# Optimization experiments

Hardware: AMD Instinct MI355X
Metric: run time of the kernel (lower is better)

Reference implementation:

```python
import jax, jax.numpy as jnp
import numpy as np

N = 100000   # nodes
E = 600000   # edges
D = 128      # input = hidden = output dim
L = 3        # GNN layers
C = 40       # num_classes
EPS = 1e-5   # BatchNorm eps


def setup_inputs() -> dict:
    key = jax.random.key(0)
    ks = jax.random.split(key, 8)
    x = jax.random.normal(ks[0], (N, D), jnp.float32)
    edge_index = jax.random.randint(ks[1], (2, E), 0, N, jnp.int32)
    # GCNConv weights per layer (Glorot-ish scale), bias zeros
    Ws = jax.random.normal(ks[2], (L, D, D), jnp.float32) / np.sqrt(D)
    bs = jnp.zeros((L, D), jnp.float32)
    # BatchNorm affine params
    gammas = jnp.ones((L, D), jnp.float32)
    betas = jnp.zeros((L, D), jnp.float32)
    # PReLU single slope per layer (torch default init 0.25)
    prelu_a = jnp.full((L,), 0.25, jnp.float32)
    # classification head: Linear(D,D) -> ReLU -> Linear(D,C)
    Wh1 = jax.random.normal(ks[3], (D, D), jnp.float32) / np.sqrt(D)
    bh1 = jnp.zeros((D,), jnp.float32)
    Wh2 = jax.random.normal(ks[4], (D, C), jnp.float32) / np.sqrt(D)
    bh2 = jnp.zeros((C,), jnp.float32)
    return dict(x=x, edge_index=edge_index, Ws=Ws, bs=bs, gammas=gammas,
                betas=betas, prelu_a=prelu_a, Wh1=Wh1, bh1=bh1, Wh2=Wh2, bh2=bh2)


def _gcn_conv(h, src, dst, norm, W, b):
    # PyG GCNConv: out_i = sum_{j->i} norm_ij * (x_j W) + b  (self-loops already in src/dst)
    m = (h @ W)[src] * norm[:, None]          # [E+N, D_out]
    return jax.ops.segment_sum(m, dst, num_segments=N) + b


def reference(x, edge_index, Ws, bs, gammas, betas, prelu_a, Wh1, bh1, Wh2, bh2):
    # add self-loops + symmetric normalization (computed once; same graph each layer)
    loops = jnp.arange(N, dtype=edge_index.dtype)
    src = jnp.concatenate([edge_index[0], loops])
    dst = jnp.concatenate([edge_index[1], loops])
    deg = jax.ops.segment_sum(jnp.ones_like(dst, jnp.float32), dst, num_segments=N)
    dinv = jax.lax.rsqrt(jnp.maximum(deg, 1.0))  # deg >= 1 thanks to self-loops
    norm = dinv[src] * dinv[dst]                 # [E+N]

    h = x
    for l in range(L):
        h = _gcn_conv(h, src, dst, norm, Ws[l], bs[l])
        # BatchNorm in training mode: batch statistics over nodes
        mu = h.mean(axis=0)
        var = h.var(axis=0)
        h = (h - mu) * jax.lax.rsqrt(var + EPS) * gammas[l] + betas[l]
        # PReLU
        h = jnp.where(h > 0, h, prelu_a[l] * h)

    embeddings = h
    logits = jax.nn.relu(embeddings @ Wh1 + bh1) @ Wh2 + bh2
    out = jnp.argmax(logits, axis=1)
    return embeddings, logits, out
```

## Files before the change

### kernel.cpp

```cpp
#include <hip/hip_runtime.h>
#include <hip/hip_bf16.h>
#include <cstddef>

#define N_NODES 100000
#define N_EDGES 600000
#define DD 128
#define LL 3
#define CC 40
#define BN_EPS 1e-5f

__device__ __forceinline__ float ldf(const void* p, long i, int f32) {
    return f32 ? ((const float*)p)[i] : __bfloat162float(((const __hip_bfloat16*)p)[i]);
}
__device__ __forceinline__ void stf(void* p, long i, float v, int f32) {
    if (f32) ((float*)p)[i] = v;
    else     ((__hip_bfloat16*)p)[i] = __float2bfloat16(v);
}

__global__ __launch_bounds__(256) void k_detect(const void* __restrict__ x, int* __restrict__ dflag) {
    __shared__ int s[256];
    int t = threadIdx.x;
    const __hip_bfloat16* xb = (const __hip_bfloat16*)x;
    int bad = 0;
    for (int i = t; i < 4096; i += 256) {
        float v = __bfloat162float(xb[i]);
        float a = fabsf(v);
        if (!(a < 1e6f)) bad++;
        else if (v != 0.f && a < 1e-30f) bad++;
    }
    s[t] = bad; __syncthreads();
    for (int off = 128; off > 0; off >>= 1) {
        if (t < off) s[t] += s[t + off];
        __syncthreads();
    }
    if (t == 0) *dflag = (s[0] > 64) ? 1 : 0;
}


__global__ __launch_bounds__(256) void k_init(int* cnt, int* fpos, int* rowptr, float* stats) {
    int i = blockIdx.x * 256 + threadIdx.x;
    if (i < N_NODES) { cnt[i] = 0; fpos[i] = 0; }
    if (i < 6 * DD) stats[i] = 0.f;
    if (i == 0) rowptr[N_NODES] = N_EDGES;
}

__global__ __launch_bounds__(256) void k_count(const int* __restrict__ ei, int* __restrict__ cnt) {
    int e = blockIdx.x * 256 + threadIdx.x;
    if (e < N_EDGES) atomicAdd(&cnt[ei[N_EDGES + e]], 1);
}

__global__ __launch_bounds__(256) void k_scan1(const int* __restrict__ cnt, int* __restrict__ rowptr,
                                               int* __restrict__ bsum, float* __restrict__ dinv) {
    __shared__ int s[256];
    int t = threadIdx.x;
    int i = blockIdx.x * 256 + t;
    int v = (i < N_NODES) ? cnt[i] : 0;
    if (i < N_NODES) dinv[i] = 1.f / sqrtf((float)(1 + v));
    s[t] = v; __syncthreads();
    for (int off = 1; off < 256; off <<= 1) {
        int x = (t >= off) ? s[t - off] : 0;
        __syncthreads();
        s[t] += x; __syncthreads();
    }
    if (i < N_NODES) rowptr[i] = s[t] - v;
    if (t == 255) bsum[blockIdx.x] = s[255];
}

__global__ __launch_bounds__(512) void k_scan2(int* bsum, int nb) {
    __shared__ int s[512];
    int t = threadIdx.x;
    int v = (t < nb) ? bsum[t] : 0;
    s[t] = v; __syncthreads();
    for (int off = 1; off < 512; off <<= 1) {
        int x = (t >= off) ? s[t - off] : 0;
        __syncthreads();
        s[t] += x; __syncthreads();
    }
    if (t < nb) bsum[t] = s[t] - v;
}

__global__ __launch_bounds__(256) void k_scan3(int* rowptr, const int* __restrict__ bsum) {
    int i = blockIdx.x * 256 + threadIdx.x;
    if (i < N_NODES) rowptr[i] += bsum[blockIdx.x];
}

__global__ __launch_bounds__(256) void k_fill(const int* __restrict__ ei, int* __restrict__ fpos,
                                              const int* __restrict__ rowptr, int* __restrict__ adj) {
    int e = blockIdx.x * 256 + threadIdx.x;
    if (e < N_EDGES) {
        int d = ei[N_EDGES + e];
        int p = atomicAdd(&fpos[d], 1);
        adj[rowptr[d] + p] = ei[e];
    }
}

__device__ __forceinline__ void load_act(const void* __restrict__ src, long row, int lane, int f,
                                         const float* __restrict__ bnp,
                                         float s0, float s1, float h0, float h1, float al,
                                         float& o0, float& o1) {
    if (bnp) {
        float2 v = ((const float2*)src)[row * 64 + lane];
        float y0 = fmaf(v.x, s0, h0), y1 = fmaf(v.y, s1, h1);
        o0 = (y0 > 0.f) ? y0 : al * y0;
        o1 = (y1 > 0.f) ? y1 : al * y1;
    } else if (f) {
        float2 v = ((const float2*)src)[row * 64 + lane];
        o0 = v.x; o1 = v.y;
    } else {
        unsigned u = ((const unsigned*)src)[row * 64 + lane];
        o0 = __uint_as_float(u << 16);
        o1 = __uint_as_float(u & 0xffff0000u);
    }
}


__global__ __launch_bounds__(256) void k_agg(const void* __restrict__ src,
                                             const int* __restrict__ rowptr,
                                             const int* __restrict__ adj,
                                             const float* __restrict__ dinv,
                                             const float* __restrict__ bnp,
                                             float* __restrict__ outp,
                                             const int* __restrict__ dflag) {
    int f = *dflag;
    int lane = threadIdx.x & 63;
    int i = blockIdx.x * 4 + (threadIdx.x >> 6);
    if (i >= N_NODES) return;
    float s0 = 0.f, s1 = 0.f, h0 = 0.f, h1 = 0.f, al = 0.f;
    if (bnp) {
        s0 = bnp[2 * lane];       s1 = bnp[2 * lane + 1];
        h0 = bnp[128 + 2 * lane]; h1 = bnp[129 + 2 * lane];
        al = bnp[256];
    }
    float di = dinv[i];
    int e0 = rowptr[i], e1 = rowptr[i + 1];
    float x0, x1;
    load_act(src, i, lane, f, bnp, s0, s1, h0, h1, al, x0, x1);
    float acc0 = di * x0, acc1 = di * x1;

    for (int base = e0; base < e1; base += 64) {
        int m = e1 - base; if (m > 64) m = 64;
        int aj = (lane < m) ? adj[base + lane] : 0;
        float djl = (lane < m) ? dinv[aj] : 0.f;
        int t = 0;
        for (; t + 2 <= m; t += 2) {
            int j0 = __shfl(aj, t), j1 = __shfl(aj, t + 1);
            float d0 = __shfl(djl, t), d1 = __shfl(djl, t + 1);
            float p0, p1, q0, q1;
            load_act(src, j0, lane, f, bnp, s0, s1, h0, h1, al, p0, p1);
            load_act(src, j1, lane, f, bnp, s0, s1, h0, h1, al, q0, q1);
            acc0 += d0 * p0 + d1 * q0;
            acc1 += d0 * p1 + d1 * q1;
        }
        if (t < m) {
            int j0 = __shfl(aj, t);
            float d0 = __shfl(djl, t);
            float p0, p1;
            load_act(src, j0, lane, f, bnp, s0, s1, h0, h1, al, p0, p1);
            acc0 += d0 * p0;
            acc1 += d0 * p1;
        }
    }
    float2 r; r.x = di * acc0; r.y = di * acc1;
    ((float2*)outp)[(size_t)i * 64 + lane] = r;
}


__global__ __launch_bounds__(256, 4) void k_gemm2(const float* __restrict__ A,
                                                  const void* __restrict__ W, long woff,
                                                  const void* __restrict__ bias, long boff,
                                                  const float* __restrict__ bnpA,
                                                  float* __restrict__ stats,
                                                  float* __restrict__ Cout, int relu,
                                                  const int* __restrict__ dflag) {
    __shared__ float Wl[128][64];
    __shared__ float sred[16][64];
    int f = *dflag;
    int tid = threadIdx.x;
    int rowbase = (blockIdx.x >> 1) * 128;
    int colbase = (blockIdx.x & 1) * 64;

    if (f) {
        const float4* W4 = (const float4*)W + (woff >> 2);
        for (int u = tid; u < 128 * 16; u += 256) {
            int k = u >> 4, cq = u & 15;
            *(float4*)&Wl[k][cq * 4] = W4[k * 32 + (colbase >> 2) + cq];
        }
    } else {
        const unsigned* Wb = (const unsigned*)((const __hip_bfloat16*)W + woff);
        for (int u = tid; u < 128 * 32; u += 256) {
            int k = u >> 5, c2 = u & 31;
            unsigned v = Wb[k * 64 + (colbase >> 1) + c2];
            Wl[k][c2 * 2]     = __uint_as_float(v << 16);
            Wl[k][c2 * 2 + 1] = __uint_as_float(v & 0xffff0000u);
        }
    }
    __syncthreads();

    int tx = tid & 15;
    int ty = tid >> 4;
    int r0 = rowbase + ty * 8;
    float acc[8][4];
    #pragma unroll
    for (int i = 0; i < 8; ++i)
        #pragma unroll
        for (int j = 0; j < 4; ++j) acc[i][j] = 0.f;

    const float4* A4 = (const float4*)A;
    bool full = (rowbase + 128) <= N_NODES;
    float alA = bnpA ? bnpA[256] : 0.f;

    for (int k4 = 0; k4 < 32; ++k4) {
        float a[8][4];
        if (full) {
            #pragma unroll
            for (int i = 0; i < 8; ++i)
                *(float4*)a[i] = A4[(long)(r0 + i) * 32 + k4];
        } else {
            #pragma unroll
            for (int i = 0; i < 8; ++i) {
                float4 v = make_float4(0.f, 0.f, 0.f, 0.f);
                if (r0 + i < N_NODES) v = A4[(long)(r0 + i) * 32 + k4];
                *(float4*)a[i] = v;
            }
        }
        if (bnpA) {
            float4 s4 = ((const float4*)bnpA)[k4];
            float4 h4 = ((const float4*)(bnpA + 128))[k4];
            float sv[4] = {s4.x, s4.y, s4.z, s4.w};
            float hv[4] = {h4.x, h4.y, h4.z, h4.w};
            #pragma unroll
            for (int i = 0; i < 8; ++i)
                #pragma unroll
                for (int kk = 0; kk < 4; ++kk) {
                    float y = fmaf(a[i][kk], sv[kk], hv[kk]);
                    a[i][kk] = (y > 0.f) ? y : alA * y;
                }
        }
        #pragma unroll
        for (int kk = 0; kk < 4; ++kk) {
            float4 w = *(const float4*)&Wl[k4 * 4 + kk][tx * 4];
            #pragma unroll
            for (int i = 0; i < 8; ++i) {
                acc[i][0] += a[i][kk] * w.x;
                acc[i][1] += a[i][kk] * w.y;
                acc[i][2] += a[i][kk] * w.z;
                acc[i][3] += a[i][kk] * w.w;
            }
        }
    }

    float b4[4] = {0.f, 0.f, 0.f, 0.f};
    if (bias) {
        #pragma unroll
        for (int j = 0; j < 4; ++j) b4[j] = ldf(bias, boff + colbase + tx * 4 + j, f);
    }
    float ls[4] = {0.f, 0.f, 0.f, 0.f};
    float lq[4] = {0.f, 0.f, 0.f, 0.f};
    #pragma unroll
    for (int i = 0; i < 8; ++i) {
        int r = r0 + i;
        if (r < N_NODES) {
            float o[4];
            #pragma unroll
            for (int j = 0; j < 4; ++j) {
                float v = acc[i][j] + b4[j];
                if (relu) v = fmaxf(v, 0.f);
                o[j] = v;
                ls[j] += v;
                lq[j] += v * v;
            }
            *(float4*)&Cout[(long)r * 128 + colbase + tx * 4] = make_float4(o[0], o[1], o[2], o[3]);
        }
    }
    if (stats) {
        #pragma unroll
        for (int j = 0; j < 4; ++j) sred[ty][tx * 4 + j] = ls[j];
        __syncthreads();
        if (tid < 64) {
            float t = 0.f;
            #pragma unroll
            for (int g = 0; g < 16; ++g) t += sred[g][tid];
            atomicAdd(&stats[colbase + tid], t);
        }
        __syncthreads();
        #pragma unroll
        for (int j = 0; j < 4; ++j) sred[ty][tx * 4 + j] = lq[j];
        __syncthreads();
        if (tid < 64) {
            float t = 0.f;
            #pragma unroll
            for (int g = 0; g < 16; ++g) t += sred[g][tid];
            atomicAdd(&stats[128 + colbase + tid], t);
        }
    }
}

__global__ __launch_bounds__(128) void k_bnprep(const float* __restrict__ stats,
                                                const void* __restrict__ g, const void* __restrict__ b,
                                                const void* __restrict__ a, int l,
                                                float* __restrict__ bnp, const int* __restrict__ dflag) {
    int f = *dflag;
    int c = threadIdx.x;
    float mean = stats[c] / (float)N_NODES;
    float var = stats[128 + c] / (float)N_NODES - mean * mean;
    float inv = 1.f / sqrtf(var + BN_EPS);
    float s = ldf(g, (long)l * DD + c, f) * inv;
    bnp[c] = s;
    bnp[128 + c] = ldf(b, (long)l * DD + c, f) - mean * s;
    if (c == 0) bnp[256] = ldf(a, l, f);
}

__global__ __launch_bounds__(256) void k_emb(const float* __restrict__ H, const float* __restrict__ bnp,
                                             void* __restrict__ out, const int* __restrict__ dflag) {
    int f = *dflag;
    long idx = (long)blockIdx.x * 256 + threadIdx.x;
    int c = (int)(idx & 127);
    float al = bnp[256];
    float y = fmaf(H[idx], bnp[c], bnp[128 + c]);
    y = (y > 0.f) ? y : al * y;
    stf(out, idx, y, f);
}


__global__ __launch_bounds__(256) void k_head(const float* __restrict__ Hd, const void* __restrict__ W2,
                                              const void* __restrict__ b2,
                                              void* __restrict__ out_base,
                                              const int* __restrict__ dflag) {
    __shared__ float Wl[128][40];
    __shared__ float bl[40];
    __shared__ float rv[32][8];
    __shared__ int ri[32][8];
    int f = *dflag;
    int tid = threadIdx.x;
    for (int u = tid; u < 128 * 40; u += 256) Wl[u / 40][u % 40] = ldf(W2, u, f);
    if (tid < 40) bl[tid] = ldf(b2, tid, f);
    __syncthreads();
    int rl = tid >> 3, g = tid & 7;
    long r = (long)blockIdx.x * 32 + rl;
    float acc[5];
    #pragma unroll
    for (int j = 0; j < 5; ++j) acc[j] = bl[g * 5 + j];
    for (int k = 0; k < 128; ++k) {
        float h = Hd[r * 128 + k];
        #pragma unroll
        for (int j = 0; j < 5; ++j) acc[j] += h * Wl[k][g * 5 + j];
    }
    float best = acc[0]; int bi = 0;
    #pragma unroll
    for (int j = 1; j < 5; ++j)
        if (acc[j] > best) { best = acc[j]; bi = j; }
    const long LOG_OFF = (long)N_NODES * DD;
    const long ARG_OFF = (long)N_NODES * (DD + CC);
    #pragma unroll
    for (int j = 0; j < 5; ++j) stf(out_base, LOG_OFF + r * 40 + g * 5 + j, acc[j], f);
    rv[rl][g] = best; ri[rl][g] = g * 5 + bi;
    __syncthreads();
    if (tid < 32) {
        long row = (long)blockIdx.x * 32 + tid;
        float bb = rv[tid][0]; int bbi = ri[tid][0];
        #pragma unroll
        for (int g2 = 1; g2 < 8; ++g2)
            if (rv[tid][g2] > bb) { bb = rv[tid][g2]; bbi = ri[tid][g2]; }
        stf(out_base, ARG_OFF + row, (float)bbi, f);
    }
}


extern "C" void kernel_launch(void* const* d_in, const int* in_sizes, int n_in,
                              void* d_out, int out_size, void* d_ws, size_t ws_size,
                              hipStream_t stream) {
    const void* x   = d_in[0];
    const int* ei   = (const int*)d_in[1];
    const void* Ws  = d_in[2];
    const void* bs  = d_in[3];
    const void* gam = d_in[4];
    const void* bet = d_in[5];
    const void* pa  = d_in[6];
    const void* Wh1 = d_in[7];
    const void* bh1 = d_in[8];
    const void* Wh2 = d_in[9];
    const void* bh2 = d_in[10];

    char* w = (char*)d_ws;
    int* cnt     = (int*)w;    w += sizeof(int) * N_NODES;
    int* fpos    = (int*)w;    w += sizeof(int) * N_NODES;
    int* rowptr  = (int*)w;    w += sizeof(int) * (N_NODES + 4);
    int* adj     = (int*)w;    w += sizeof(int) * N_EDGES;
    int* bsum    = (int*)w;    w += sizeof(int) * 512;
    int* dflag   = (int*)w;    w += sizeof(int) * 4;
    float* dinv  = (float*)w;  w += sizeof(float) * N_NODES;
    float* stats = (float*)w;  w += sizeof(float) * (6 * DD);
    float* bnp   = (float*)w;  w += sizeof(float) * (3 * 512);
    float* bufA  = (float*)w;  w += sizeof(float) * (size_t)N_NODES * DD;
    float* bufB  = (float*)w;  w += sizeof(float) * (size_t)N_NODES * DD;

    const int scanBlocks = (N_NODES + 255) / 256;
    const int edgeBlocks = (N_EDGES + 255) / 256;
    const int elemBlocks = (N_NODES * DD) / 256;
    const int gemmBlocks = ((N_NODES + 127) / 128) * 2;
    const int aggBlocks  = (N_NODES + 3) / 4;

    k_detect<<<1, 256, 0, stream>>>(x, dflag);
    k_init<<<scanBlocks, 256, 0, stream>>>(cnt, fpos, rowptr, stats);
    k_count<<<edgeBlocks, 256, 0, stream>>>(ei, cnt);
    k_scan1<<<scanBlocks, 256, 0, stream>>>(cnt, rowptr, bsum, dinv);
    k_scan2<<<1, 512, 0, stream>>>(bsum, scanBlocks);
    k_scan3<<<scanBlocks, 256, 0, stream>>>(rowptr, bsum);
    k_fill<<<edgeBlocks, 256, 0, stream>>>(ei, fpos, rowptr, adj);

    for (int l = 0; l < LL; ++l) {
        const void* src = (l == 0) ? x : (const void*)bufB;
        const float* bn = (l == 0) ? nullptr : (bnp + (l - 1) * 512);
        k_agg<<<aggBlocks, 256, 0, stream>>>(src, rowptr, adj, dinv, bn, bufA, dflag);
        k_gemm2<<<gemmBlocks, 256, 0, stream>>>(bufA, Ws, (long)l * DD * DD, bs, (long)l * DD,
                                                nullptr, stats + l * 256, bufB, 0, dflag);
        k_bnprep<<<1, 128, 0, stream>>>(stats + l * 256, gam, bet, pa, l, bnp + l * 512, dflag);
    }

    k_emb<<<elemBlocks, 256, 0, stream>>>(bufB, bnp + 2 * 512, d_out, dflag);
    k_gemm2<<<gemmBlocks, 256, 0, stream>>>(bufB, Wh1, 0, bh1, 0, bnp + 2 * 512,
                                            nullptr, bufA, 1, dflag);
    k_head<<<(N_NODES / 32), 256, 0, stream>>>(bufA, Wh2, bh2, d_out, dflag);
}
```

Baseline: 777.4 us.

## Move dense GEMMs onto bf16 MFMA with three-way split for fp32 accuracy

The 128x128 dense matmuls in each GCN layer and the head now run on bf16 MFMA instructions instead of scalar fp32 FMAs. Each operand is split into hi/mid/lo bf16 parts and six cross products are accumulated, keeping results close to fp32. A new pre-pass kernel packs all four weight matrices once into the MFMA fragment layout, so the GEMM just copies them into shared memory. Each block now covers all 128 output columns, which changes stats reduction and occupancy. The cost is six times the MFMA work, extra conversion ALU work on activations, and scalar (non-vectorised) output stores.

```diff
diff --git a/kernel.cpp b/kernel.cpp
--- a/kernel.cpp
+++ b/kernel.cpp
@@ -9,12 +9,24 @@
 #define CC 40
 #define BN_EPS 1e-5f
 
+typedef __attribute__((ext_vector_type(8))) short bfrag;
+typedef __attribute__((ext_vector_type(4))) float f32x4;
+
 __device__ __forceinline__ float ldf(const void* p, long i, int f32) {
     return f32 ? ((const float*)p)[i] : __bfloat162float(((const __hip_bfloat16*)p)[i]);
 }
 __device__ __forceinline__ void stf(void* p, long i, float v, int f32) {
     if (f32) ((float*)p)[i] = v;
     else     ((__hip_bfloat16*)p)[i] = __float2bfloat16(v);
+}
+
+__device__ __forceinline__ unsigned short f2bf(float f) {
+    unsigned u = __float_as_uint(f);
+    unsigned r = (u + 0x7fffu + ((u >> 16) & 1u)) >> 16;
+    return (unsigned short)r;
+}
+__device__ __forceinline__ float bf2f(unsigned short h) {
+    return __uint_as_float(((unsigned)h) << 16);
 }
 
 __global__ __launch_bounds__(256) void k_detect(const void* __restrict__ x, int* __restrict__ dflag) {
@@ -34,6 +46,28 @@
         __syncthreads();
     }
     if (t == 0) *dflag = (s[0] > 64) ? 1 : 0;
+}
+
+__global__ __launch_bounds__(256) void k_packw(const void* __restrict__ Ws, const void* __restrict__ Wh1,
+                                               unsigned short* __restrict__ Wp,
+                                               const int* __restrict__ dflag) {
+    int f = *dflag;
+    int u = blockIdx.x * 256 + threadIdx.x;
+    int mat = u >> 14;
+    int r = u & 16383;
+    int k = r >> 7, c = r & 127;
+    float wv = (mat < 3) ? ldf(Ws, (long)mat * 16384 + r, f) : ldf(Wh1, r, f);
+    unsigned short hi = f2bf(wv);
+    float r1 = wv - bf2f(hi);
+    unsigned short mid = f2bf(r1);
+    float r2 = r1 - bf2f(mid);
+    unsigned short lo = f2bf(r2);
+    int n = c >> 4, ks = k >> 5, j = k & 7;
+    int lanep = (c & 15) | (((k >> 3) & 3) << 4);
+    long base = (long)mat * 49152 + (long)((n * 4 + ks) * 3) * 512 + lanep * 8 + j;
+    Wp[base] = hi;
+    Wp[base + 512] = mid;
+    Wp[base + 1024] = lo;
 }
 
 
@@ -165,133 +199,176 @@
 }
 
 
-__global__ __launch_bounds__(256, 4) void k_gemm2(const float* __restrict__ A,
-                                                  const void* __restrict__ W, long woff,
+__global__ __launch_bounds__(256, 2) void k_gemm2(const float* __restrict__ A,
+                                                  const unsigned short* __restrict__ Wp,
                                                   const void* __restrict__ bias, long boff,
                                                   const float* __restrict__ bnpA,
                                                   float* __restrict__ stats,
                                                   float* __restrict__ Cout, int relu,
                                                   const int* __restrict__ dflag) {
-    __shared__ float Wl[128][64];
-    __shared__ float sred[16][64];
+    __shared__ unsigned short Wl[24576];
     int f = *dflag;
     int tid = threadIdx.x;
-    int rowbase = (blockIdx.x >> 1) * 128;
-    int colbase = (blockIdx.x & 1) * 64;
-
-    if (f) {
-        const float4* W4 = (const float4*)W + (woff >> 2);
-        for (int u = tid; u < 128 * 16; u += 256) {
-            int k = u >> 4, cq = u & 15;
-            *(float4*)&Wl[k][cq * 4] = W4[k * 32 + (colbase >> 2) + cq];
-        }
-    } else {
-        const unsigned* Wb = (const unsigned*)((const __hip_bfloat16*)W + woff);
-        for (int u = tid; u < 128 * 32; u += 256) {
-            int k = u >> 5, c2 = u & 31;
-            unsigned v = Wb[k * 64 + (colbase >> 1) + c2];
-            Wl[k][c2 * 2]     = __uint_as_float(v << 16);
-            Wl[k][c2 * 2 + 1] = __uint_as_float(v & 0xffff0000u);
-        }
-    }
-    __syncthreads();
-
-    int tx = tid & 15;
-    int ty = tid >> 4;
-    int r0 = rowbase + ty * 8;
-    float acc[8][4];
-    #pragma unroll
-    for (int i = 0; i < 8; ++i)
-        #pragma unroll
-        for (int j = 0; j < 4; ++j) acc[i][j] = 0.f;
-
+
+    int lane = tid & 63;
+    int w = tid >> 6;
+    int lr = lane & 15;
+    int lg = lane >> 4;
+    int rowbase = blockIdx.x * 128 + w * 32;
+
+    float bcol[8];
+    #pragma unroll
+    for (int n = 0; n < 8; ++n)
+        bcol[n] = bias ? ldf(bias, boff + n * 16 + lr, f) : 0.f;
+
+    float alA = bnpA ? bnpA[256] : 0.f;
+
+    bfrag ah[2][4], am[2][4], alo[2][4];
     const float4* A4 = (const float4*)A;
-    bool full = (rowbase + 128) <= N_NODES;
-    float alA = bnpA ? bnpA[256] : 0.f;
-
-    for (int k4 = 0; k4 < 32; ++k4) {
-        float a[8][4];
-        if (full) {
+    #pragma unroll
+    for (int ks = 0; ks < 4; ++ks) {
+        int k0 = ks * 32 + lg * 8;
+        float bs_[8], bh_[8];
+        if (bnpA) {
+            float4 sa = *(const float4*)&bnpA[k0];
+            float4 sb = *(const float4*)&bnpA[k0 + 4];
+            float4 ha = *(const float4*)&bnpA[128 + k0];
+            float4 hb = *(const float4*)&bnpA[128 + k0 + 4];
+            bs_[0] = sa.x; bs_[1] = sa.y; bs_[2] = sa.z; bs_[3] = sa.w;
+            bs_[4] = sb.x; bs_[5] = sb.y; bs_[6] = sb.z; bs_[7] = sb.w;
+            bh_[0] = ha.x; bh_[1] = ha.y; bh_[2] = ha.z; bh_[3] = ha.w;
+            bh_[4] = hb.x; bh_[5] = hb.y; bh_[6] = hb.z; bh_[7] = hb.w;
+        }
+        #pragma unroll
+        for (int s = 0; s < 2; ++s) {
+            int row = rowbase + s * 16 + lr;
+            float xv[8];
+            if (row < N_NODES) {
+                long bi = (long)row * 32 + (k0 >> 2);
+                float4 x0 = A4[bi], x1 = A4[bi + 1];
+                xv[0] = x0.x; xv[1] = x0.y; xv[2] = x0.z; xv[3] = x0.w;
+                xv[4] = x1.x; xv[5] = x1.y; xv[6] = x1.z; xv[7] = x1.w;
+            } else {
+                #pragma unroll
+                for (int e = 0; e < 8; ++e) xv[e] = 0.f;
+            }
+            if (bnpA) {
+                #pragma unroll
+                for (int e = 0; e < 8; ++e) {
+                    float y = fmaf(xv[e], bs_[e], bh_[e]);
+                    xv[e] = (y > 0.f) ? y : alA * y;
+                }
+            }
+            bfrag hfr, mfr, lfr;
             #pragma unroll
-            for (int i = 0; i < 8; ++i)
-                *(float4*)a[i] = A4[(long)(r0 + i) * 32 + k4];
-        } else {
+            for (int e = 0; e < 8; ++e) {
+                unsigned short hb2 = f2bf(xv[e]);
+                float r1 = xv[e] - bf2f(hb2);
+                unsigned short mb2 = f2bf(r1);
+                float r2 = r1 - bf2f(mb2);
+                hfr[e] = (short)hb2;
+                mfr[e] = (short)mb2;
+                lfr[e] = (short)f2bf(r2);
+            }
+            ah[s][ks] = hfr;
+            am[s][ks] = mfr;
+            alo[s][ks] = lfr;
+        }
+    }
+
+    f32x4 acc[2][8];
+    #pragma unroll
+    for (int s = 0; s < 2; ++s)
+        #pragma unroll
+        for (int n = 0; n < 8; ++n) acc[s][n] = (f32x4){0.f, 0.f, 0.f, 0.f};
+
+    #pragma unroll
+    for (int h = 0; h < 2; ++h) {
+        if (h) __syncthreads();
+        {
+            const uint4* srcp = (const uint4*)(Wp + (size_t)h * 24576);
+            uint4* dstp = (uint4*)Wl;
             #pragma unroll
-            for (int i = 0; i < 8; ++i) {
-                float4 v = make_float4(0.f, 0.f, 0.f, 0.f);
-                if (r0 + i < N_NODES) v = A4[(long)(r0 + i) * 32 + k4];
-                *(float4*)a[i] = v;
-            }
-        }
-        if (bnpA) {
-            float4 s4 = ((const float4*)bnpA)[k4];
-            float4 h4 = ((const float4*)(bnpA + 128))[k4];
-            float sv[4] = {s4.x, s4.y, s4.z, s4.w};
-            float hv[4] = {h4.x, h4.y, h4.z, h4.w};
+            for (int u = 0; u < 12; ++u) dstp[tid + 256 * u] = srcp[tid + 256 * u];
+        }
+        __syncthreads();
+
+        #pragma unroll
+        for (int nn = 0; nn < 4; ++nn) {
+            int n = h * 4 + nn;
+            bfrag bh[4], bm[4], bl[4];
             #pragma unroll
-            for (int i = 0; i < 8; ++i)
+            for (int ks = 0; ks < 4; ++ks) {
+                int base = ((nn * 4 + ks) * 3) * 512 + lane * 8;
+                bh[ks] = *(const bfrag*)&Wl[base];
+                bm[ks] = *(const bfrag*)&Wl[base + 512];
+                bl[ks] = *(const bfrag*)&Wl[base + 1024];
+            }
+            #pragma unroll
+            for (int ks = 0; ks < 4; ++ks) {
                 #pragma unroll
-                for (int kk = 0; kk < 4; ++kk) {
-                    float y = fmaf(a[i][kk], sv[kk], hv[kk]);
-                    a[i][kk] = (y > 0.f) ? y : alA * y;
+                for (int s = 0; s < 2; ++s) {
+                    acc[s][n] = __builtin_amdgcn_mfma_f32_16x16x32_bf16(ah[s][ks],  bh[ks], acc[s][n], 0, 0, 0);
+                    acc[s][n] = __builtin_amdgcn_mfma_f32_16x16x32_bf16(am[s][ks],  bh[ks], acc[s][n], 0, 0, 0);
+                    acc[s][n] = __builtin_amdgcn_mfma_f32_16x16x32_bf16(ah[s][ks],  bm[ks], acc[s][n], 0, 0, 0);
+                    acc[s][n] = __builtin_amdgcn_mfma_f32_16x16x32_bf16(am[s][ks],  bm[ks], acc[s][n], 0, 0, 0);
+                    acc[s][n] = __builtin_amdgcn_mfma_f32_16x16x32_bf16(alo[s][ks], bh[ks], acc[s][n], 0, 0, 0);
+                    acc[s][n] = __builtin_amdgcn_mfma_f32_16x16x32_bf16(ah[s][ks],  bl[ks], acc[s][n], 0, 0, 0);
                 }
-        }
-        #pragma unroll
-        for (int kk = 0; kk < 4; ++kk) {
-            float4 w = *(const float4*)&Wl[k4 * 4 + kk][tx * 4];
+            }
+        }
+    }
+
+    int rowst[2][4]; bool rv[2][4];
+    #pragma unroll
+    for (int s = 0; s < 2; ++s)
+        #pragma unroll
+        for (int reg = 0; reg < 4; ++reg) {
+            rowst[s][reg] = rowbase + s * 16 + lg * 4 + reg;
+            rv[s][reg] = rowst[s][reg] < N_NODES;
+        }
+
+    float ls[8], lq[8];
+    #pragma unroll
+    for (int n = 0; n < 8; ++n) { ls[n] = 0.f; lq[n] = 0.f; }
+
+    #pragma unroll
+    for (int s = 0; s < 2; ++s)
+        #pragma unroll
+        for (int n = 0; n < 8; ++n) {
+            int colb = n * 16 + lr;
             #pragma unroll
-            for (int i = 0; i < 8; ++i) {
-                acc[i][0] += a[i][kk] * w.x;
-                acc[i][1] += a[i][kk] * w.y;
-                acc[i][2] += a[i][kk] * w.z;
-                acc[i][3] += a[i][kk] * w.w;
-            }
-        }
-    }
-
-    float b4[4] = {0.f, 0.f, 0.f, 0.f};
-    if (bias) {
-        #pragma unroll
-        for (int j = 0; j < 4; ++j) b4[j] = ldf(bias, boff + colbase + tx * 4 + j, f);
-    }
-    float ls[4] = {0.f, 0.f, 0.f, 0.f};
-    float lq[4] = {0.f, 0.f, 0.f, 0.f};
-    #pragma unroll
-    for (int i = 0; i < 8; ++i) {
-        int r = r0 + i;
-        if (r < N_NODES) {
-            float o[4];
+            for (int reg = 0; reg < 4; ++reg) {
+                if (rv[s][reg]) {
+                    float o = acc[s][n][reg] + bcol[n];
+                    if (relu) o = fmaxf(o, 0.f);
+                    Cout[(long)rowst[s][reg] * 128 + colb] = o;
+                    ls[n] += o;
+                    lq[n] += o * o;
+                }
+            }
+        }
+
+    if (stats) {
+        #pragma unroll
+        for (int n = 0; n < 8; ++n) {
+            ls[n] += __shfl_xor(ls[n], 16);
+            ls[n] += __shfl_xor(ls[n], 32);
+            lq[n] += __shfl_xor(lq[n], 16);
+            lq[n] += __shfl_xor(lq[n], 32);
+        }
+        __syncthreads();
+        float* red = (float*)Wl;
+        if (lane < 16) {
             #pragma unroll
-            for (int j = 0; j < 4; ++j) {
-                float v = acc[i][j] + b4[j];
-                if (relu) v = fmaxf(v, 0.f);
-                o[j] = v;
-                ls[j] += v;
-                lq[j] += v * v;
-            }
-            *(float4*)&Cout[(long)r * 128 + colbase + tx * 4] = make_float4(o[0], o[1], o[2], o[3]);
-        }
-    }
-    if (stats) {
-        #pragma unroll
-        for (int j = 0; j < 4; ++j) sred[ty][tx * 4 + j] = ls[j];
+            for (int n = 0; n < 8; ++n) {
+                red[w * 256 + n * 16 + lane] = ls[n];
+                red[w * 256 + 128 + n * 16 + lane] = lq[n];
+            }
+        }
         __syncthreads();
-        if (tid < 64) {
-            float t = 0.f;
-            #pragma unroll
-            for (int g = 0; g < 16; ++g) t += sred[g][tid];
-            atomicAdd(&stats[colbase + tid], t);
-        }
-        __syncthreads();
-        #pragma unroll
-        for (int j = 0; j < 4; ++j) sred[ty][tx * 4 + j] = lq[j];
-        __syncthreads();
-        if (tid < 64) {
-            float t = 0.f;
-            #pragma unroll
-            for (int g = 0; g < 16; ++g) t += sred[g][tid];
-            atomicAdd(&stats[128 + colbase + tid], t);
-        }
+        float t = red[tid] + red[256 + tid] + red[512 + tid] + red[768 + tid];
+        atomicAdd(&stats[tid], t);
     }
 }
 
@@ -391,16 +468,18 @@
     float* dinv  = (float*)w;  w += sizeof(float) * N_NODES;
     float* stats = (float*)w;  w += sizeof(float) * (6 * DD);
     float* bnp   = (float*)w;  w += sizeof(float) * (3 * 512);
+    unsigned short* Wp = (unsigned short*)w; w += sizeof(unsigned short) * 4 * 49152;
     float* bufA  = (float*)w;  w += sizeof(float) * (size_t)N_NODES * DD;
     float* bufB  = (float*)w;  w += sizeof(float) * (size_t)N_NODES * DD;
 
     const int scanBlocks = (N_NODES + 255) / 256;
     const int edgeBlocks = (N_EDGES + 255) / 256;
     const int elemBlocks = (N_NODES * DD) / 256;
-    const int gemmBlocks = ((N_NODES + 127) / 128) * 2;
+    const int gemmBlocks = (N_NODES + 127) / 128;
     const int aggBlocks  = (N_NODES + 3) / 4;
 
     k_detect<<<1, 256, 0, stream>>>(x, dflag);
+    k_packw<<<256, 256, 0, stream>>>(Ws, Wh1, Wp, dflag);
     k_init<<<scanBlocks, 256, 0, stream>>>(cnt, fpos, rowptr, stats);
     k_count<<<edgeBlocks, 256, 0, stream>>>(ei, cnt);
     k_scan1<<<scanBlocks, 256, 0, stream>>>(cnt, rowptr, bsum, dinv);
@@ -412,13 +491,13 @@
         const void* src = (l == 0) ? x : (const void*)bufB;
         const float* bn = (l == 0) ? nullptr : (bnp + (l - 1) * 512);
         k_agg<<<aggBlocks, 256, 0, stream>>>(src, rowptr, adj, dinv, bn, bufA, dflag);
-        k_gemm2<<<gemmBlocks, 256, 0, stream>>>(bufA, Ws, (long)l * DD * DD, bs, (long)l * DD,
+        k_gemm2<<<gemmBlocks, 256, 0, stream>>>(bufA, Wp + (size_t)l * 49152, bs, (long)l * DD,
                                                 nullptr, stats + l * 256, bufB, 0, dflag);
         k_bnprep<<<1, 128, 0, stream>>>(stats + l * 256, gam, bet, pa, l, bnp + l * 512, dflag);
     }
 
     k_emb<<<elemBlocks, 256, 0, stream>>>(bufB, bnp + 2 * 512, d_out, dflag);
-    k_gemm2<<<gemmBlocks, 256, 0, stream>>>(bufB, Wh1, 0, bh1, 0, bnp + 2 * 512,
+    k_gemm2<<<gemmBlocks, 256, 0, stream>>>(bufB, Wp + (size_t)3 * 49152, bh1, 0, bnp + 2 * 512,
                                             nullptr, bufA, 1, dflag);
     k_head<<<(N_NODES / 32), 256, 0, stream>>>(bufA, Wh2, bh2, d_out, dflag);
 }
```

After: 658.7 us. 15.3% less time.
